# Optimization experiments

Measured on AMD Instinct MI355X. Metric: run time of the kernel, lower is better.

Reference implementation:

```python
import jax, jax.numpy as jnp
import numpy as np

N = 50000      # nodes
E = 800000     # edges
C = 128        # feature width (in = hidden = out)
H = 2          # attention heads
ATT_SLOPE = 0.2   # GATConv leaky_relu slope
OUT_SLOPE = 0.01  # F.leaky_relu_ default slope


def setup_inputs() -> dict:
    key = jax.random.key(0)
    ks = jax.random.split(key, 12)
    s = 1.0 / np.sqrt(C)
    inp = {
        "x": jax.random.normal(ks[0], (N, C), jnp.float32),
        "edge_index": jax.random.randint(ks[1], (2, E), 0, N, dtype=jnp.int32),
        "edge_attr": jax.random.normal(ks[2], (E, C), jnp.float32),
        # GATConv layer 1 params (lin weight, att_src, att_dst, bias)
        "W1": jax.random.normal(ks[3], (C, H * C), jnp.float32) * s,
        "a_src1": jax.random.normal(ks[4], (H, C), jnp.float32) * s,
        "a_dst1": jax.random.normal(ks[5], (H, C), jnp.float32) * s,
        "b1": jnp.zeros((C,), jnp.float32),
        # GATConv layer 2 params
        "W2": jax.random.normal(ks[6], (C, H * C), jnp.float32) * s,
        "a_src2": jax.random.normal(ks[7], (H, C), jnp.float32) * s,
        "a_dst2": jax.random.normal(ks[8], (H, C), jnp.float32) * s,
        "b2": jnp.zeros((C,), jnp.float32),
    }
    return inp


def _segment_softmax(alpha, dst, n):
    # alpha: [E', H]; softmax over edges sharing the same dst node
    amax = jax.ops.segment_max(alpha, dst, num_segments=n)
    amax = jnp.where(jnp.isfinite(amax), amax, 0.0)
    ex = jnp.exp(alpha - amax[dst])
    denom = jax.ops.segment_sum(ex, dst, num_segments=n)
    return ex / (denom[dst] + 1e-16)


def _gat_layer(x, src, dst, W, a_s, a_d, b):
    # GATConv, concat=False (mean over heads), edge_dim=None, eval mode
    n = x.shape[0]
    xp = (x @ W).reshape(n, H, C)                  # [N,H,C]
    a_i = jnp.sum(xp * a_s, axis=-1)               # [N,H] src scores
    a_j = jnp.sum(xp * a_d, axis=-1)               # [N,H] dst scores
    e = jax.nn.leaky_relu(a_i[src] + a_j[dst], ATT_SLOPE)   # [E',H]
    att = _segment_softmax(e, dst, n)              # [E',H]
    msg = att[:, :, None] * xp[src]                # [E',H,C]
    out = jax.ops.segment_sum(msg, dst, num_segments=n)     # [N,H,C]
    return out.mean(axis=1) + b                    # concat=False -> mean heads


def reference(x, edge_index, edge_attr, W1, a_src1, a_dst1, b1,
              W2, a_src2, a_dst2, b2):
    src0, dst0 = edge_index[0], edge_index[1]
    loop = jnp.arange(x.shape[0], dtype=edge_index.dtype)
    src = jnp.concatenate([src0, loop])            # add self loops
    dst = jnp.concatenate([dst0, loop])
    score = None
    for (W, a_s, a_d, b) in ((W1, a_src1, a_dst1, b1),
                             (W2, a_src2, a_dst2, b2)):
        x = _gat_layer(x, src, dst, W, a_s, a_d, b)
        # edge score uses pre-activation x (leaky_relu_ happens after the gather)
        score = jnp.sum(x[src0] * x[dst0] * edge_attr, axis=-1)  # [E]
        x = jax.nn.leaky_relu(x, OUT_SLOPE)
        score = jax.nn.sigmoid(score)
    return x, score
```

## Files before the change

kernel.cpp:

```cpp
#include <hip/hip_runtime.h>
#include <hip/hip_bf16.h>
#include <hip/hip_fp16.h>

#define NN 50000
#define EE 800000
#define CC 128
#define HH 2
#define ATT_SLOPE 0.2f
#define OUT_SLOPE 0.01f

__device__ __forceinline__ float lrelu(float v, float s) {
    return v > 0.0f ? v : s * v;
}

__device__ __forceinline__ float4 ld_half4(const __half* p) {
    uint2 u = *(const uint2*)p;
    float2 fa = __half22float2(*reinterpret_cast<const __half2*>(&u.x));
    float2 fb = __half22float2(*reinterpret_cast<const __half2*>(&u.y));
    return make_float4(fa.x, fa.y, fb.x, fb.y);
}


__global__ void zero_kernel(int* __restrict__ p, int n) {
    int i = blockIdx.x * blockDim.x + threadIdx.x;
    if (i < n) p[i] = 0;
}

__global__ void count_kernel(const int* __restrict__ dst, int* __restrict__ cnt,
                             int E, int N) {
    int i = blockIdx.x * blockDim.x + threadIdx.x;
    int total = E + N;
    if (i >= total) return;
    int d = (i < E) ? dst[i] : (i - E);
    atomicAdd(&cnt[d], 1);
}

__global__ __launch_bounds__(256) void bsum_kernel(const int* __restrict__ cnt,
                                                   int* __restrict__ bsum, int n) {
    __shared__ int sh[4];
    int i = blockIdx.x * 256 + threadIdx.x;
    int v = (i < n) ? cnt[i] : 0;
    #pragma unroll
    for (int off = 32; off; off >>= 1) v += __shfl_xor(v, off);
    if ((threadIdx.x & 63) == 0) sh[threadIdx.x >> 6] = v;
    __syncthreads();
    if (threadIdx.x == 0) bsum[blockIdx.x] = sh[0] + sh[1] + sh[2] + sh[3];
}

__global__ __launch_bounds__(256) void bscan_kernel(int* __restrict__ bsum, int nb) {
    __shared__ int buf[2][256];
    int t = threadIdx.x;
    int v = (t < nb) ? bsum[t] : 0;
    buf[0][t] = v;
    __syncthreads();
    int cur = 0;
    for (int off = 1; off < 256; off <<= 1) {
        int nxt = cur ^ 1;
        int add = (t >= off) ? buf[cur][t - off] : 0;
        buf[nxt][t] = buf[cur][t] + add;
        __syncthreads();
        cur = nxt;
    }
    if (t < nb) bsum[t] = buf[cur][t] - v;
}

__global__ __launch_bounds__(256) void scan2_kernel(const int* __restrict__ cnt,
                                                    const int* __restrict__ boff,
                                                    int* __restrict__ rowptr,
                                                    int* __restrict__ fillptr, int n) {
    __shared__ int buf[2][256];
    int t = threadIdx.x;
    int i = blockIdx.x * 256 + t;
    int v = (i < n) ? cnt[i] : 0;
    buf[0][t] = v;
    __syncthreads();
    int cur = 0;
    for (int off = 1; off < 256; off <<= 1) {
        int nxt = cur ^ 1;
        int add = (t >= off) ? buf[cur][t - off] : 0;
        buf[nxt][t] = buf[cur][t] + add;
        __syncthreads();
        cur = nxt;
    }
    int excl = buf[cur][t] - v + boff[blockIdx.x];
    if (i < n) { rowptr[i] = excl; fillptr[i] = excl; }
    if (i == n - 1) rowptr[n] = excl + v;
}

__global__ void scatter_kernel(const int* __restrict__ src, const int* __restrict__ dst,
                               int* __restrict__ fillptr, int* __restrict__ col,
                               int E, int N) {
    int i = blockIdx.x * blockDim.x + threadIdx.x;
    int total = E + N;
    if (i >= total) return;
    int s, d;
    if (i < E) { s = src[i]; d = dst[i]; }
    else       { s = d = i - E; }
    int pos = atomicAdd(&fillptr[d], 1);
    col[pos] = s;
}


#define BM 128
#define BK 32

#define FMA8(i, ac, bb0, bb1) \
    acc[i][0] += ac * bb0.x; acc[i][1] += ac * bb0.y; acc[i][2] += ac * bb0.z; acc[i][3] += ac * bb0.w; \
    acc[i][4] += ac * bb1.x; acc[i][5] += ac * bb1.y; acc[i][6] += ac * bb1.z; acc[i][7] += ac * bb1.w;

__global__ __launch_bounds__(256) void gemm_kernel(const float* __restrict__ X,
                            const float* __restrict__ W,
                            const float* __restrict__ a_src,
                            const float* __restrict__ a_dst,
                            __half* __restrict__ XP,
                            float* __restrict__ a4,
                            int M) {
    __shared__ float As[BM][BK + 4];
    __shared__ float Bs[BK][128 + 4];
    int m0 = blockIdx.x * BM;
    int h  = blockIdx.y;
    int n0 = h << 7;
    int t  = threadIdx.x;
    int tx = t & 15;
    int ty = t >> 4;

    float acc[8][8] = {};

    for (int kt = 0; kt < CC; kt += BK) {
        #pragma unroll
        for (int j = 0; j < 4; ++j) {
            int idx = t + j * 256;
            int row = idx >> 3;
            int kq  = idx & 7;
            float4 v = make_float4(0.f, 0.f, 0.f, 0.f);
            if (m0 + row < M)
                v = *(const float4*)(X + (size_t)(m0 + row) * CC + kt + kq * 4);
            *(float4*)(&As[row][kq * 4]) = v;
        }
        #pragma unroll
        for (int j = 0; j < 4; ++j) {
            int idx = t + j * 256;
            int k   = idx >> 5;
            int cq  = idx & 31;
            *(float4*)(&Bs[k][cq * 4]) =
                *(const float4*)(W + (size_t)(kt + k) * 256 + n0 + cq * 4);
        }
        __syncthreads();
        #pragma unroll
        for (int k0 = 0; k0 < BK; k0 += 4) {
            float4 av[8];
            #pragma unroll
            for (int i = 0; i < 8; ++i)
                av[i] = *(const float4*)(&As[ty * 8 + i][k0]);
            #pragma unroll
            for (int kk = 0; kk < 4; ++kk) {
                float4 b0 = *(const float4*)(&Bs[k0 + kk][tx * 8]);
                float4 b1 = *(const float4*)(&Bs[k0 + kk][tx * 8 + 4]);
                if (kk == 0) { FMA8(0, av[0].x, b0, b1); FMA8(1, av[1].x, b0, b1); FMA8(2, av[2].x, b0, b1); FMA8(3, av[3].x, b0, b1); FMA8(4, av[4].x, b0, b1); FMA8(5, av[5].x, b0, b1); FMA8(6, av[6].x, b0, b1); FMA8(7, av[7].x, b0, b1); }
                if (kk == 1) { FMA8(0, av[0].y, b0, b1); FMA8(1, av[1].y, b0, b1); FMA8(2, av[2].y, b0, b1); FMA8(3, av[3].y, b0, b1); FMA8(4, av[4].y, b0, b1); FMA8(5, av[5].y, b0, b1); FMA8(6, av[6].y, b0, b1); FMA8(7, av[7].y, b0, b1); }
                if (kk == 2) { FMA8(0, av[0].z, b0, b1); FMA8(1, av[1].z, b0, b1); FMA8(2, av[2].z, b0, b1); FMA8(3, av[3].z, b0, b1); FMA8(4, av[4].z, b0, b1); FMA8(5, av[5].z, b0, b1); FMA8(6, av[6].z, b0, b1); FMA8(7, av[7].z, b0, b1); }
                if (kk == 3) { FMA8(0, av[0].w, b0, b1); FMA8(1, av[1].w, b0, b1); FMA8(2, av[2].w, b0, b1); FMA8(3, av[3].w, b0, b1); FMA8(4, av[4].w, b0, b1); FMA8(5, av[5].w, b0, b1); FMA8(6, av[6].w, b0, b1); FMA8(7, av[7].w, b0, b1); }
            }
        }
        __syncthreads();
    }

    int coff = tx * 8;
    float4 as0 = *(const float4*)(a_src + h * 128 + coff);
    float4 as1 = *(const float4*)(a_src + h * 128 + coff + 4);
    float4 ad0 = *(const float4*)(a_dst + h * 128 + coff);
    float4 ad1 = *(const float4*)(a_dst + h * 128 + coff + 4);
    #pragma unroll
    for (int i = 0; i < 8; ++i) {
        int row = m0 + ty * 8 + i;
        float ps = acc[i][0] * as0.x + acc[i][1] * as0.y + acc[i][2] * as0.z + acc[i][3] * as0.w
                 + acc[i][4] * as1.x + acc[i][5] * as1.y + acc[i][6] * as1.z + acc[i][7] * as1.w;
        float pd = acc[i][0] * ad0.x + acc[i][1] * ad0.y + acc[i][2] * ad0.z + acc[i][3] * ad0.w
                 + acc[i][4] * ad1.x + acc[i][5] * ad1.y + acc[i][6] * ad1.z + acc[i][7] * ad1.w;
        #pragma unroll
        for (int off = 1; off < 16; off <<= 1) {
            ps += __shfl_xor(ps, off);
            pd += __shfl_xor(pd, off);
        }
        if (row < M) {
            __half2 h0 = __floats2half2_rn(acc[i][0], acc[i][1]);
            __half2 h1 = __floats2half2_rn(acc[i][2], acc[i][3]);
            __half2 h2 = __floats2half2_rn(acc[i][4], acc[i][5]);
            __half2 h3 = __floats2half2_rn(acc[i][6], acc[i][7]);
            uint4 pack;
            pack.x = *reinterpret_cast<unsigned*>(&h0);
            pack.y = *reinterpret_cast<unsigned*>(&h1);
            pack.z = *reinterpret_cast<unsigned*>(&h2);
            pack.w = *reinterpret_cast<unsigned*>(&h3);
            *(uint4*)(XP + (size_t)row * 256 + n0 + tx * 8) = pack;
            if (tx == 0) {
                a4[(size_t)row * 4 + h]     = ps;
                a4[(size_t)row * 4 + 2 + h] = pd;
            }
        }
    }
}

__global__ __launch_bounds__(256) void agg_kernel(const __half* __restrict__ xp,
                           const float* __restrict__ a4,
                           const int* __restrict__ rowptr,
                           const int* __restrict__ col,
                           const float* __restrict__ bias,
                           float* __restrict__ out_post,
                           __half* __restrict__ shadow,
                           int write_shadow) {
    int n = __builtin_amdgcn_readfirstlane(blockIdx.x * 4 + (int)(threadIdx.x >> 6));
    int lane = threadIdx.x & 63;
    int h = lane >> 5;
    int r0 = rowptr[n], r1 = rowptr[n + 1];
    float2 adv = *(const float2*)(a4 + (size_t)n * 4 + 2);
    float ad = h ? adv.y : adv.x;

    float denom = 0.f;
    float4 acc = make_float4(0.f, 0.f, 0.f, 0.f);

    int k = r0;
    for (; k + 3 < r1; k += 4) {
        int s0 = __builtin_amdgcn_readfirstlane(col[k]);
        int s1 = __builtin_amdgcn_readfirstlane(col[k + 1]);
        int s2 = __builtin_amdgcn_readfirstlane(col[k + 2]);
        int s3 = __builtin_amdgcn_readfirstlane(col[k + 3]);
        float2 av0 = *(const float2*)(a4 + (size_t)s0 * 4);
        float2 av1 = *(const float2*)(a4 + (size_t)s1 * 4);
        float2 av2 = *(const float2*)(a4 + (size_t)s2 * 4);
        float2 av3 = *(const float2*)(a4 + (size_t)s3 * 4);
        float4 v0 = ld_half4(xp + (size_t)s0 * 256 + lane * 4);
        float4 v1 = ld_half4(xp + (size_t)s1 * 256 + lane * 4);
        float4 v2 = ld_half4(xp + (size_t)s2 * 256 + lane * 4);
        float4 v3 = ld_half4(xp + (size_t)s3 * 256 + lane * 4);
        float e0 = lrelu((h ? av0.y : av0.x) + ad, ATT_SLOPE);
        float e1 = lrelu((h ? av1.y : av1.x) + ad, ATT_SLOPE);
        float e2 = lrelu((h ? av2.y : av2.x) + ad, ATT_SLOPE);
        float e3 = lrelu((h ? av3.y : av3.x) + ad, ATT_SLOPE);
        float x0 = __expf(e0);
        float x1 = __expf(e1);
        float x2 = __expf(e2);
        float x3 = __expf(e3);
        denom += (x0 + x1) + (x2 + x3);
        acc.x += x0 * v0.x + x1 * v1.x + x2 * v2.x + x3 * v3.x;
        acc.y += x0 * v0.y + x1 * v1.y + x2 * v2.y + x3 * v3.y;
        acc.z += x0 * v0.z + x1 * v1.z + x2 * v2.z + x3 * v3.z;
        acc.w += x0 * v0.w + x1 * v1.w + x2 * v2.w + x3 * v3.w;
    }
    for (; k < r1; ++k) {
        int s0 = __builtin_amdgcn_readfirstlane(col[k]);
        float2 av0 = *(const float2*)(a4 + (size_t)s0 * 4);
        float4 v0 = ld_half4(xp + (size_t)s0 * 256 + lane * 4);
        float e0 = lrelu((h ? av0.y : av0.x) + ad, ATT_SLOPE);
        float x0 = __expf(e0);
        denom += x0;
        acc.x += x0 * v0.x;
        acc.y += x0 * v0.y;
        acc.z += x0 * v0.z;
        acc.w += x0 * v0.w;
    }

    float inv = 1.0f / (denom + 1e-16f);
    float4 val = make_float4(acc.x * inv, acc.y * inv, acc.z * inv, acc.w * inv);
    float4 other;
    other.x = __shfl_xor(val.x, 32);
    other.y = __shfl_xor(val.y, 32);
    other.z = __shfl_xor(val.z, 32);
    other.w = __shfl_xor(val.w, 32);
    if (h == 0) {
        float4 bv = *(const float4*)(bias + lane * 4);
        float4 pre;
        pre.x = 0.5f * (val.x + other.x) + bv.x;
        pre.y = 0.5f * (val.y + other.y) + bv.y;
        pre.z = 0.5f * (val.z + other.z) + bv.z;
        pre.w = 0.5f * (val.w + other.w) + bv.w;
        float4 o;
        o.x = lrelu(pre.x, OUT_SLOPE);
        o.y = lrelu(pre.y, OUT_SLOPE);
        o.z = lrelu(pre.z, OUT_SLOPE);
        o.w = lrelu(pre.w, OUT_SLOPE);
        *(float4*)(out_post + (size_t)n * CC + lane * 4) = o;
        if (write_shadow) {
            __half2 s0 = __floats2half2_rn(pre.x, pre.y);
            __half2 s1 = __floats2half2_rn(pre.z, pre.w);
            uint2 pk;
            pk.x = *reinterpret_cast<unsigned*>(&s0);
            pk.y = *reinterpret_cast<unsigned*>(&s1);
            *(uint2*)(shadow + (size_t)n * CC + lane * 4) = pk;
        }
    }
}

__global__ __launch_bounds__(256) void score_kernel(const __half* __restrict__ xq,
                             const int* __restrict__ src,
                             const int* __restrict__ dst,
                             const float* __restrict__ ea,
                             float* __restrict__ score) {
    int e = blockIdx.x * 8 + (int)(threadIdx.x >> 5);
    int q = threadIdx.x & 31;
    int s = src[e], d = dst[e];
    float4 xs = ld_half4(xq + (size_t)s * CC + q * 4);
    float4 xd = ld_half4(xq + (size_t)d * CC + q * 4);
    float4 ev = *(const float4*)(ea + (size_t)e * CC + q * 4);
    float p = xs.x * xd.x * ev.x + xs.y * xd.y * ev.y +
              xs.z * xd.z * ev.z + xs.w * xd.w * ev.w;
    #pragma unroll
    for (int off = 16; off; off >>= 1) p += __shfl_xor(p, off);
    if (q == 0) score[e] = 1.0f / (1.0f + __expf(-p));
}

extern "C" void kernel_launch(void* const* d_in, const int* in_sizes, int n_in,
                              void* d_out, int out_size, void* d_ws, size_t ws_size,
                              hipStream_t stream) {
    (void)in_sizes; (void)n_in; (void)out_size; (void)ws_size;
    const float* x       = (const float*)d_in[0];
    const int*   eidx    = (const int*)d_in[1];
    const float* ea      = (const float*)d_in[2];
    const float* W1      = (const float*)d_in[3];
    const float* a_src1  = (const float*)d_in[4];
    const float* a_dst1  = (const float*)d_in[5];
    const float* b1      = (const float*)d_in[6];
    const float* W2      = (const float*)d_in[7];
    const float* a_src2  = (const float*)d_in[8];
    const float* a_dst2  = (const float*)d_in[9];
    const float* b2      = (const float*)d_in[10];

    const int* srcp = eidx;
    const int* dstp = eidx + EE;

    char* ws = (char*)d_ws;
    auto alloc = [&](size_t bytes) {
        char* p = ws;
        ws += (bytes + 255) & ~(size_t)255;
        return p;
    };
    const int NB = (NN + 255) / 256;
    int*    cnt     = (int*)alloc((size_t)NN * 4);
    int*    rowptr  = (int*)alloc((size_t)(NN + 1) * 4);
    int*    fillptr = (int*)alloc((size_t)NN * 4);
    int*    col     = (int*)alloc((size_t)(EE + NN) * 4);
    int*    bsum    = (int*)alloc((size_t)NB * 4);
    float*  a4      = (float*)alloc((size_t)NN * 4 * 4);
    __half* xp      = (__half*)alloc((size_t)NN * 256 * 2);
    float*  x1      = (float*)alloc((size_t)NN * CC * 4);
    __half* xq      = (__half*)alloc((size_t)NN * CC * 2);

    float* outx = (float*)d_out;
    float* outs = outx + (size_t)NN * CC;

    int total = EE + NN;

    zero_kernel<<<(NN + 255) / 256, 256, 0, stream>>>(cnt, NN);
    count_kernel<<<(total + 255) / 256, 256, 0, stream>>>(dstp, cnt, EE, NN);
    bsum_kernel<<<NB, 256, 0, stream>>>(cnt, bsum, NN);
    bscan_kernel<<<1, 256, 0, stream>>>(bsum, NB);
    scan2_kernel<<<NB, 256, 0, stream>>>(cnt, bsum, rowptr, fillptr, NN);
    scatter_kernel<<<(total + 255) / 256, 256, 0, stream>>>(srcp, dstp, fillptr, col, EE, NN);

    dim3 ggrid((NN + BM - 1) / BM, 2);

    gemm_kernel<<<ggrid, 256, 0, stream>>>(x, W1, a_src1, a_dst1, xp, a4, NN);
    agg_kernel<<<NN / 4, 256, 0, stream>>>(xp, a4, rowptr, col, b1, x1, xq, 0);

    gemm_kernel<<<ggrid, 256, 0, stream>>>(x1, W2, a_src2, a_dst2, xp, a4, NN);
    agg_kernel<<<NN / 4, 256, 0, stream>>>(xp, a4, rowptr, col, b2, outx, xq, 1);

    score_kernel<<<EE / 8, 256, 0, stream>>>(xq, srcp, dstp, ea, outs);
}
```

Before: 891.9 us.

## Use half-wave per node in aggregation and CSR-ordered score kernel

The aggregation kernel now gives each destination node 32 lanes instead of 64, with each lane loading 8 halves (16 bytes) per neighbor row. This doubles the nodes per block and widens the loads. The score kernel now walks the CSR by destination node and uses an edge-id array recorded during scatter. This keeps the destination feature row in registers, but edge_attr and score are accessed in scattered order. Writing the extra eid array costs more memory traffic in scatter, and the random edge_attr reads may hurt coalescing.

Measured after the change: 928.1 us. 4.1% more time.

```diff
diff --git a/kernel.cpp b/kernel.cpp
--- a/kernel.cpp
+++ b/kernel.cpp
@@ -89,15 +89,16 @@
 
 __global__ void scatter_kernel(const int* __restrict__ src, const int* __restrict__ dst,
                                int* __restrict__ fillptr, int* __restrict__ col,
-                               int E, int N) {
+                               int* __restrict__ eid, int E, int N) {
     int i = blockIdx.x * blockDim.x + threadIdx.x;
     int total = E + N;
     if (i >= total) return;
-    int s, d;
-    if (i < E) { s = src[i]; d = dst[i]; }
-    else       { s = d = i - E; }
+    int s, d, e;
+    if (i < E) { s = src[i]; d = dst[i]; e = i; }
+    else       { s = d = i - E; e = -1; }
     int pos = atomicAdd(&fillptr[d], 1);
     col[pos] = s;
+    eid[pos] = e;
 }
 
 
@@ -209,104 +210,147 @@
                            float* __restrict__ out_post,
                            __half* __restrict__ shadow,
                            int write_shadow) {
-    int n = __builtin_amdgcn_readfirstlane(blockIdx.x * 4 + (int)(threadIdx.x >> 6));
-    int lane = threadIdx.x & 63;
-    int h = lane >> 5;
+    int tid = threadIdx.x;
+    int n = blockIdx.x * 8 + (tid >> 5);
+    int q = tid & 31;
+    int h = q >> 4;
+    int c8 = (q & 15) * 8;
     int r0 = rowptr[n], r1 = rowptr[n + 1];
     float2 adv = *(const float2*)(a4 + (size_t)n * 4 + 2);
     float ad = h ? adv.y : adv.x;
 
     float denom = 0.f;
-    float4 acc = make_float4(0.f, 0.f, 0.f, 0.f);
+    float acc[8] = {0.f, 0.f, 0.f, 0.f, 0.f, 0.f, 0.f, 0.f};
+
+#define ACC8(u, xw) do { \
+        float2 f0 = __half22float2(*reinterpret_cast<const __half2*>(&u.x)); \
+        float2 f1 = __half22float2(*reinterpret_cast<const __half2*>(&u.y)); \
+        float2 f2 = __half22float2(*reinterpret_cast<const __half2*>(&u.z)); \
+        float2 f3 = __half22float2(*reinterpret_cast<const __half2*>(&u.w)); \
+        acc[0] += xw * f0.x; acc[1] += xw * f0.y; \
+        acc[2] += xw * f1.x; acc[3] += xw * f1.y; \
+        acc[4] += xw * f2.x; acc[5] += xw * f2.y; \
+        acc[6] += xw * f3.x; acc[7] += xw * f3.y; } while (0)
 
     int k = r0;
     for (; k + 3 < r1; k += 4) {
-        int s0 = __builtin_amdgcn_readfirstlane(col[k]);
-        int s1 = __builtin_amdgcn_readfirstlane(col[k + 1]);
-        int s2 = __builtin_amdgcn_readfirstlane(col[k + 2]);
-        int s3 = __builtin_amdgcn_readfirstlane(col[k + 3]);
+        int s0 = col[k], s1 = col[k + 1], s2 = col[k + 2], s3 = col[k + 3];
         float2 av0 = *(const float2*)(a4 + (size_t)s0 * 4);
         float2 av1 = *(const float2*)(a4 + (size_t)s1 * 4);
         float2 av2 = *(const float2*)(a4 + (size_t)s2 * 4);
         float2 av3 = *(const float2*)(a4 + (size_t)s3 * 4);
-        float4 v0 = ld_half4(xp + (size_t)s0 * 256 + lane * 4);
-        float4 v1 = ld_half4(xp + (size_t)s1 * 256 + lane * 4);
-        float4 v2 = ld_half4(xp + (size_t)s2 * 256 + lane * 4);
-        float4 v3 = ld_half4(xp + (size_t)s3 * 256 + lane * 4);
-        float e0 = lrelu((h ? av0.y : av0.x) + ad, ATT_SLOPE);
-        float e1 = lrelu((h ? av1.y : av1.x) + ad, ATT_SLOPE);
-        float e2 = lrelu((h ? av2.y : av2.x) + ad, ATT_SLOPE);
-        float e3 = lrelu((h ? av3.y : av3.x) + ad, ATT_SLOPE);
-        float x0 = __expf(e0);
-        float x1 = __expf(e1);
-        float x2 = __expf(e2);
-        float x3 = __expf(e3);
+        uint4 u0 = *(const uint4*)(xp + (size_t)s0 * 256 + q * 8);
+        uint4 u1 = *(const uint4*)(xp + (size_t)s1 * 256 + q * 8);
+        uint4 u2 = *(const uint4*)(xp + (size_t)s2 * 256 + q * 8);
+        uint4 u3 = *(const uint4*)(xp + (size_t)s3 * 256 + q * 8);
+        float x0 = __expf(lrelu((h ? av0.y : av0.x) + ad, ATT_SLOPE));
+        float x1 = __expf(lrelu((h ? av1.y : av1.x) + ad, ATT_SLOPE));
+        float x2 = __expf(lrelu((h ? av2.y : av2.x) + ad, ATT_SLOPE));
+        float x3 = __expf(lrelu((h ? av3.y : av3.x) + ad, ATT_SLOPE));
         denom += (x0 + x1) + (x2 + x3);
-        acc.x += x0 * v0.x + x1 * v1.x + x2 * v2.x + x3 * v3.x;
-        acc.y += x0 * v0.y + x1 * v1.y + x2 * v2.y + x3 * v3.y;
-        acc.z += x0 * v0.z + x1 * v1.z + x2 * v2.z + x3 * v3.z;
-        acc.w += x0 * v0.w + x1 * v1.w + x2 * v2.w + x3 * v3.w;
+        ACC8(u0, x0); ACC8(u1, x1); ACC8(u2, x2); ACC8(u3, x3);
     }
     for (; k < r1; ++k) {
-        int s0 = __builtin_amdgcn_readfirstlane(col[k]);
+        int s0 = col[k];
         float2 av0 = *(const float2*)(a4 + (size_t)s0 * 4);
-        float4 v0 = ld_half4(xp + (size_t)s0 * 256 + lane * 4);
-        float e0 = lrelu((h ? av0.y : av0.x) + ad, ATT_SLOPE);
-        float x0 = __expf(e0);
+        uint4 u0 = *(const uint4*)(xp + (size_t)s0 * 256 + q * 8);
+        float x0 = __expf(lrelu((h ? av0.y : av0.x) + ad, ATT_SLOPE));
         denom += x0;
-        acc.x += x0 * v0.x;
-        acc.y += x0 * v0.y;
-        acc.z += x0 * v0.z;
-        acc.w += x0 * v0.w;
-    }
+        ACC8(u0, x0);
+    }
+#undef ACC8
 
     float inv = 1.0f / (denom + 1e-16f);
-    float4 val = make_float4(acc.x * inv, acc.y * inv, acc.z * inv, acc.w * inv);
-    float4 other;
-    other.x = __shfl_xor(val.x, 32);
-    other.y = __shfl_xor(val.y, 32);
-    other.z = __shfl_xor(val.z, 32);
-    other.w = __shfl_xor(val.w, 32);
+    float v[8], o[8];
+    #pragma unroll
+    for (int j = 0; j < 8; ++j) v[j] = acc[j] * inv;
+    #pragma unroll
+    for (int j = 0; j < 8; ++j) o[j] = __shfl_xor(v[j], 16);
     if (h == 0) {
-        float4 bv = *(const float4*)(bias + lane * 4);
-        float4 pre;
-        pre.x = 0.5f * (val.x + other.x) + bv.x;
-        pre.y = 0.5f * (val.y + other.y) + bv.y;
-        pre.z = 0.5f * (val.z + other.z) + bv.z;
-        pre.w = 0.5f * (val.w + other.w) + bv.w;
-        float4 o;
-        o.x = lrelu(pre.x, OUT_SLOPE);
-        o.y = lrelu(pre.y, OUT_SLOPE);
-        o.z = lrelu(pre.z, OUT_SLOPE);
-        o.w = lrelu(pre.w, OUT_SLOPE);
-        *(float4*)(out_post + (size_t)n * CC + lane * 4) = o;
+        float4 b0 = *(const float4*)(bias + c8);
+        float4 b1 = *(const float4*)(bias + c8 + 4);
+        float pre[8];
+        pre[0] = 0.5f * (v[0] + o[0]) + b0.x;
+        pre[1] = 0.5f * (v[1] + o[1]) + b0.y;
+        pre[2] = 0.5f * (v[2] + o[2]) + b0.z;
+        pre[3] = 0.5f * (v[3] + o[3]) + b0.w;
+        pre[4] = 0.5f * (v[4] + o[4]) + b1.x;
+        pre[5] = 0.5f * (v[5] + o[5]) + b1.y;
+        pre[6] = 0.5f * (v[6] + o[6]) + b1.z;
+        pre[7] = 0.5f * (v[7] + o[7]) + b1.w;
+        float4 p0 = make_float4(lrelu(pre[0], OUT_SLOPE), lrelu(pre[1], OUT_SLOPE),
+                                lrelu(pre[2], OUT_SLOPE), lrelu(pre[3], OUT_SLOPE));
+        float4 p1 = make_float4(lrelu(pre[4], OUT_SLOPE), lrelu(pre[5], OUT_SLOPE),
+                                lrelu(pre[6], OUT_SLOPE), lrelu(pre[7], OUT_SLOPE));
+        *(float4*)(out_post + (size_t)n * CC + c8)     = p0;
+        *(float4*)(out_post + (size_t)n * CC + c8 + 4) = p1;
         if (write_shadow) {
-            __half2 s0 = __floats2half2_rn(pre.x, pre.y);
-            __half2 s1 = __floats2half2_rn(pre.z, pre.w);
-            uint2 pk;
+            __half2 s0 = __floats2half2_rn(pre[0], pre[1]);
+            __half2 s1 = __floats2half2_rn(pre[2], pre[3]);
+            __half2 s2 = __floats2half2_rn(pre[4], pre[5]);
+            __half2 s3 = __floats2half2_rn(pre[6], pre[7]);
+            uint4 pk;
             pk.x = *reinterpret_cast<unsigned*>(&s0);
             pk.y = *reinterpret_cast<unsigned*>(&s1);
-            *(uint2*)(shadow + (size_t)n * CC + lane * 4) = pk;
+            pk.z = *reinterpret_cast<unsigned*>(&s2);
+            pk.w = *reinterpret_cast<unsigned*>(&s3);
+            *(uint4*)(shadow + (size_t)n * CC + c8) = pk;
         }
     }
 }
 
 __global__ __launch_bounds__(256) void score_kernel(const __half* __restrict__ xq,
-                             const int* __restrict__ src,
-                             const int* __restrict__ dst,
+                             const int* __restrict__ rowptr,
+                             const int* __restrict__ col,
+                             const int* __restrict__ eid,
                              const float* __restrict__ ea,
                              float* __restrict__ score) {
-    int e = blockIdx.x * 8 + (int)(threadIdx.x >> 5);
-    int q = threadIdx.x & 31;
-    int s = src[e], d = dst[e];
-    float4 xs = ld_half4(xq + (size_t)s * CC + q * 4);
-    float4 xd = ld_half4(xq + (size_t)d * CC + q * 4);
-    float4 ev = *(const float4*)(ea + (size_t)e * CC + q * 4);
-    float p = xs.x * xd.x * ev.x + xs.y * xd.y * ev.y +
-              xs.z * xd.z * ev.z + xs.w * xd.w * ev.w;
-    #pragma unroll
-    for (int off = 16; off; off >>= 1) p += __shfl_xor(p, off);
-    if (q == 0) score[e] = 1.0f / (1.0f + __expf(-p));
+    int tid = threadIdx.x;
+    int n = blockIdx.x * 8 + (tid >> 5);
+    int q = tid & 31;
+    int r0 = rowptr[n], r1 = rowptr[n + 1];
+    float4 xd = ld_half4(xq + (size_t)n * CC + q * 4);
+
+    int k = r0;
+    for (; k + 1 < r1; k += 2) {
+        int e0 = eid[k], e1 = eid[k + 1];
+        int s0 = col[k], s1 = col[k + 1];
+        float4 xs0 = ld_half4(xq + (size_t)s0 * CC + q * 4);
+        float4 xs1 = ld_half4(xq + (size_t)s1 * CC + q * 4);
+        float p0 = 0.f, p1 = 0.f;
+        if (e0 >= 0) {
+            float4 ev = *(const float4*)(ea + (size_t)e0 * CC + q * 4);
+            p0 = xs0.x * xd.x * ev.x + xs0.y * xd.y * ev.y +
+                 xs0.z * xd.z * ev.z + xs0.w * xd.w * ev.w;
+        }
+        if (e1 >= 0) {
+            float4 ev = *(const float4*)(ea + (size_t)e1 * CC + q * 4);
+            p1 = xs1.x * xd.x * ev.x + xs1.y * xd.y * ev.y +
+                 xs1.z * xd.z * ev.z + xs1.w * xd.w * ev.w;
+        }
+        #pragma unroll
+        for (int off = 16; off; off >>= 1) {
+            p0 += __shfl_xor(p0, off);
+            p1 += __shfl_xor(p1, off);
+        }
+        if (q == 0) {
+            if (e0 >= 0) score[e0] = 1.0f / (1.0f + __expf(-p0));
+            if (e1 >= 0) score[e1] = 1.0f / (1.0f + __expf(-p1));
+        }
+    }
+    if (k < r1) {
+        int e0 = eid[k];
+        if (e0 >= 0) {
+            int s0 = col[k];
+            float4 xs0 = ld_half4(xq + (size_t)s0 * CC + q * 4);
+            float4 ev = *(const float4*)(ea + (size_t)e0 * CC + q * 4);
+            float p0 = xs0.x * xd.x * ev.x + xs0.y * xd.y * ev.y +
+                       xs0.z * xd.z * ev.z + xs0.w * xd.w * ev.w;
+            #pragma unroll
+            for (int off = 16; off; off >>= 1) p0 += __shfl_xor(p0, off);
+            if (q == 0) score[e0] = 1.0f / (1.0f + __expf(-p0));
+        }
+    }
 }
 
 extern "C" void kernel_launch(void* const* d_in, const int* in_sizes, int n_in,
@@ -339,6 +383,7 @@
     int*    rowptr  = (int*)alloc((size_t)(NN + 1) * 4);
     int*    fillptr = (int*)alloc((size_t)NN * 4);
     int*    col     = (int*)alloc((size_t)(EE + NN) * 4);
+    int*    eid     = (int*)alloc((size_t)(EE + NN) * 4);
     int*    bsum    = (int*)alloc((size_t)NB * 4);
     float*  a4      = (float*)alloc((size_t)NN * 4 * 4);
     __half* xp      = (__half*)alloc((size_t)NN * 256 * 2);
@@ -355,15 +400,15 @@
     bsum_kernel<<<NB, 256, 0, stream>>>(cnt, bsum, NN);
     bscan_kernel<<<1, 256, 0, stream>>>(bsum, NB);
     scan2_kernel<<<NB, 256, 0, stream>>>(cnt, bsum, rowptr, fillptr, NN);
-    scatter_kernel<<<(total + 255) / 256, 256, 0, stream>>>(srcp, dstp, fillptr, col, EE, NN);
+    scatter_kernel<<<(total + 255) / 256, 256, 0, stream>>>(srcp, dstp, fillptr, col, eid, EE, NN);
 
     dim3 ggrid((NN + BM - 1) / BM, 2);
 
     gemm_kernel<<<ggrid, 256, 0, stream>>>(x, W1, a_src1, a_dst1, xp, a4, NN);
-    agg_kernel<<<NN / 4, 256, 0, stream>>>(xp, a4, rowptr, col, b1, x1, xq, 0);
+    agg_kernel<<<NN / 8, 256, 0, stream>>>(xp, a4, rowptr, col, b1, x1, xq, 0);
 
     gemm_kernel<<<ggrid, 256, 0, stream>>>(x1, W2, a_src2, a_dst2, xp, a4, NN);
-    agg_kernel<<<NN / 4, 256, 0, stream>>>(xp, a4, rowptr, col, b2, outx, xq, 1);
-
-    score_kernel<<<EE / 8, 256, 0, stream>>>(xq, srcp, dstp, ea, outs);
-}
+    agg_kernel<<<NN / 8, 256, 0, stream>>>(xp, a4, rowptr, col, b2, outx, xq, 1);
+
+    score_kernel<<<NN / 8, 256, 0, stream>>>(xq, rowptr, col, eid, ea, outs);
+}
```
